# Performance work log

Measured on AMD Instinct MI355X. Metric: run time of the kernel, lower is better.

## Reference

```python
import jax, jax.numpy as jnp
import numpy as np

EPS = 1e-5


def conv2d(x, w, b, pad, mode='reflect'):
    # x: [B,C,H,W], w: [O,I,kh,kw]
    if pad > 0:
        x = jnp.pad(x, ((0, 0), (0, 0), (pad, pad), (pad, pad)), mode=mode)
    y = jax.lax.conv_general_dilated(x, w, (1, 1), 'VALID',
                                     dimension_numbers=('NCHW', 'OIHW', 'NCHW'))
    return y + b[None, :, None, None]


def inorm(x):
    # InstanceNorm2d, no affine (nn.InstanceNorm2d default)
    m = jnp.mean(x, axis=(2, 3), keepdims=True)
    v = jnp.mean((x - m) ** 2, axis=(2, 3), keepdims=True)
    return (x - m) * jax.lax.rsqrt(v + EPS)


def upsample2(x):
    # nn.Upsample(scale_factor=2), default nearest
    return jnp.repeat(jnp.repeat(x, 2, axis=2), 2, axis=3)


def bilinear_sample(img, py, px):
    # img [B,C,H,W]; py/px [B,H,W] float coords; zero padding outside bounds
    B, C, H, W = img.shape
    y0 = jnp.floor(py)
    x0 = jnp.floor(px)
    wy1 = (py - y0)[:, None]
    wx1 = (px - x0)[:, None]
    wy0 = 1.0 - wy1
    wx0 = 1.0 - wx1
    y0i = y0.astype(jnp.int32)
    x0i = x0.astype(jnp.int32)
    flat = img.reshape(B, C, H * W)

    def tap(yi, xi):
        valid = (yi >= 0) & (yi < H) & (xi >= 0) & (xi < W)
        idx = jnp.clip(yi, 0, H - 1) * W + jnp.clip(xi, 0, W - 1)
        g = jnp.take_along_axis(flat, idx.reshape(B, 1, H * W), axis=2).reshape(B, C, H, W)
        return g * valid[:, None]

    return (tap(y0i, x0i) * wy0 * wx0 + tap(y0i, x0i + 1) * wy0 * wx1 +
            tap(y0i + 1, x0i) * wy1 * wx0 + tap(y0i + 1, x0i + 1) * wy1 * wx1)


def mdcn(x, offset, mask, w, b):
    # modulated deformable conv v2: 3x3, stride 1, pad 1, 1 deformable group
    # offset [B,18,H,W] read as interleaved (dy,dx) per kernel tap; mask [B,9,H,W]
    B, C, H, W = x.shape
    off = offset.reshape(B, 9, 2, H, W)
    base_y = jnp.arange(H, dtype=x.dtype)[None, :, None]
    base_x = jnp.arange(W, dtype=x.dtype)[None, None, :]
    cols = []
    for k in range(9):
        ky, kx = k // 3 - 1, k % 3 - 1
        py = base_y + ky + off[:, k, 0]
        px = base_x + kx + off[:, k, 1]
        cols.append(bilinear_sample(x, py, px) * mask[:, k][:, None])
    col = jnp.stack(cols, axis=2)  # [B,C,9,H,W]
    out = jnp.einsum('bckhw,ock->bohw', col, w.reshape(w.shape[0], C, 9))
    return out + b[None, :, None, None]


def dcn_block(out, skip, off_w, off_b, w, b):
    # ModulatedDeformConvPack(double=True): offsets from concat, deform conv on skip
    dc = jnp.concatenate([out, skip], axis=1)
    om = conv2d(dc, off_w, off_b, 1, mode='constant')
    o1, o2, m = jnp.split(om, 3, axis=1)
    offset = jnp.concatenate([o1, o2], axis=1)
    pre = mdcn(skip, offset, jax.nn.sigmoid(m), w, b)
    return jnp.concatenate([pre, out], axis=1), offset


def decoder_fwd(x, skip1, skip2,
                rb0_w1, rb0_b1, rb0_w2, rb0_b2,
                rb1_w1, rb1_b1, rb1_w2, rb1_b2,
                conv1_w, conv1_b, conv3_w, conv3_b,
                conv5_w, conv5_b, conv6_w, conv6_b,
                dcn2_off_w, dcn2_off_b, dcn2_w, dcn2_b,
                dcn1_off_w, dcn1_off_b, dcn1_w, dcn1_b):
    out = x
    # i=0: ResBlocks (2 resblocks, 'in' norm, relu, reflect pad)
    for (w1, b1, w2, b2) in ((rb0_w1, rb0_b1, rb0_w2, rb0_b2),
                             (rb1_w1, rb1_b1, rb1_w2, rb1_b2)):
        h = jax.nn.relu(inorm(conv2d(out, w1, b1, 1)))
        out = out + inorm(conv2d(h, w2, b2, 1))
    # i=1: Conv2dBlock(256->256, 5x5)
    out = jax.nn.relu(inorm(conv2d(out, conv1_w, conv1_b, 2)))
    # dcn_2 hook (baseline_idx=2 -> dcn_idx=[1,3])
    out, offset2 = dcn_block(out, skip2, dcn2_off_w, dcn2_off_b, dcn2_w, dcn2_b)
    # i=2: upsample
    out = upsample2(out)
    # i=3: Conv2dBlock(512->128, 5x5)
    out = jax.nn.relu(inorm(conv2d(out, conv3_w, conv3_b, 2)))
    # dcn hook
    out, offset1 = dcn_block(out, skip1, dcn1_off_w, dcn1_off_b, dcn1_w, dcn1_b)
    # i=4: upsample
    out = upsample2(out)
    # i=5: Conv2dBlock(256->64, 5x5)
    out = jax.nn.relu(inorm(conv2d(out, conv5_w, conv5_b, 2)))
    # i=6: Conv2dBlock(64->3, 7x7, no norm, tanh)
    out = jnp.tanh(conv2d(out, conv6_w, conv6_b, 3))
    offset_sum = 0.5 * (jnp.mean(jnp.abs(offset1)) + jnp.mean(jnp.abs(offset2)))
    return out, offset_sum


def setup_inputs() -> dict:
    key = jax.random.key(0)
    ks = iter(jax.random.split(key, 48))

    def randn(shape, scale=1.0):
        return jax.random.normal(next(ks), shape, dtype=jnp.float32) * scale

    def conv_w(o, i, k, scale=1.0):
        return randn((o, i, k, k), scale / float(np.sqrt(i * k * k)))

    d = {}
    d['x'] = randn((8, 256, 32, 32))
    d['skip1'] = randn((8, 128, 64, 64))
    d['skip2'] = randn((8, 256, 32, 32))
    for r in range(2):
        d[f'rb{r}_w1'] = conv_w(256, 256, 3)
        d[f'rb{r}_b1'] = randn((256,), 0.01)
        d[f'rb{r}_w2'] = conv_w(256, 256, 3)
        d[f'rb{r}_b2'] = randn((256,), 0.01)
    d['conv1_w'] = conv_w(256, 256, 5); d['conv1_b'] = randn((256,), 0.01)
    d['conv3_w'] = conv_w(128, 512, 5); d['conv3_b'] = randn((128,), 0.01)
    d['conv5_w'] = conv_w(64, 256, 5); d['conv5_b'] = randn((64,), 0.01)
    d['conv6_w'] = conv_w(3, 64, 7); d['conv6_b'] = randn((3,), 0.01)
    d['dcn2_off_w'] = conv_w(27, 512, 3, 0.1); d['dcn2_off_b'] = randn((27,), 0.01)
    d['dcn2_w'] = conv_w(256, 256, 3); d['dcn2_b'] = randn((256,), 0.01)
    d['dcn1_off_w'] = conv_w(27, 256, 3, 0.1); d['dcn1_off_b'] = randn((27,), 0.01)
    d['dcn1_w'] = conv_w(128, 128, 3); d['dcn1_b'] = randn((128,), 0.01)
    return d


def reference(x, skip1, skip2,
              rb0_w1, rb0_b1, rb0_w2, rb0_b2,
              rb1_w1, rb1_b1, rb1_w2, rb1_b2,
              conv1_w, conv1_b, conv3_w, conv3_b,
              conv5_w, conv5_b, conv6_w, conv6_b,
              dcn2_off_w, dcn2_off_b, dcn2_w, dcn2_b,
              dcn1_off_w, dcn1_off_b, dcn1_w, dcn1_b):
    return decoder_fwd(x, skip1, skip2,
                       rb0_w1, rb0_b1, rb0_w2, rb0_b2,
                       rb1_w1, rb1_b1, rb1_w2, rb1_b2,
                       conv1_w, conv1_b, conv3_w, conv3_b,
                       conv5_w, conv5_b, conv6_w, conv6_b,
                       dcn2_off_w, dcn2_off_b, dcn2_w, dcn2_b,
                       dcn1_off_w, dcn1_off_b, dcn1_w, dcn1_b)
```

## Files before the change

### kernel.cpp

```cpp
#include <hip/hip_runtime.h>
#include <hip/hip_bf16.h>
#include <math.h>

typedef __hip_bfloat16 bf16;
typedef unsigned short u16;
typedef __attribute__((ext_vector_type(8))) short short8;
typedef __attribute__((ext_vector_type(4))) float f32x4;

__device__ __forceinline__ float LD(const float* p) { return *p; }
__device__ __forceinline__ float LD(const bf16* p)  { return __bfloat162float(*p); }
__device__ __forceinline__ void  ST(float* p, float v) { *p = v; }
__device__ __forceinline__ void  ST(bf16* p, float v)  { *p = __float2bfloat16(v); }
__device__ __forceinline__ u16   f2b(float v) { bf16 h = __float2bfloat16(v); return *reinterpret_cast<u16*>(&h); }
__device__ __forceinline__ float b2fu(u16 u) { bf16 h = *reinterpret_cast<bf16*>(&u); return __bfloat162float(h); }

__global__ __launch_bounds__(256) void copy_kernel(const float* __restrict__ in,
                                                   float* __restrict__ out, int n) {
    int i = blockIdx.x * blockDim.x + threadIdx.x;
    if (i < n) out[i] = in[i];
}

__global__ __launch_bounds__(256) void wsplit_kernel(const float* __restrict__ w,
                                                     u16* __restrict__ hi, u16* __restrict__ lo,
                                                     int O, int C, int KK)
{
    const int i = blockIdx.x * 256 + threadIdx.x;
    const int n = O * C * KK;
    if (i >= n) return;
    const int o = i / (C * KK);
    const int r = i - o * C * KK;
    const int c = r / KK;
    const int t = r - c * KK;
    const float v = w[i];
    const bf16 h = __float2bfloat16(v);
    const float hv = __bfloat162float(h);
    const bf16 l = __float2bfloat16(v - hv);
    const size_t dst = ((size_t)t * O + o) * C + c;
    hi[dst] = *(const u16*)&h;
    lo[dst] = *(const u16*)&l;
}

__global__ __launch_bounds__(256) void wsplit2_kernel(const float* __restrict__ w,
                                                      u16* __restrict__ hi, u16* __restrict__ lo,
                                                      int O, int C, int KK)
{
    const int i = blockIdx.x * 256 + threadIdx.x;
    const int n = O * C * KK;
    if (i >= n) return;
    const int o = i / (C * KK);
    const int r = i - o * C * KK;
    const int c = r / KK;
    const int t = r - c * KK;
    const float v = w[i];
    const bf16 h = __float2bfloat16(v);
    const float hv = __bfloat162float(h);
    const bf16 l = __float2bfloat16(v - hv);
    const int nch = C >> 5;
    const int cc = c >> 5, quad = (c >> 3) & 3, q = c & 7;
    const size_t dst = ((((size_t)t * nch + cc) * 4 + quad) * O + o) * 8 + q;
    hi[dst] = *(const u16*)&h;
    lo[dst] = *(const u16*)&l;
}

template<typename T1, typename T2, int K, bool UP, int EPI, bool ASPLIT,
         int NR, int NCOL, int MT, int MW>
__global__ __launch_bounds__(MW * 128) void conv_mfma3(
        const T1* __restrict__ src1, const T2* __restrict__ src2,
        int C1, int C,
        const u16* __restrict__ wth, const u16* __restrict__ wtl,
        const float* __restrict__ bias,
        void* __restrict__ outv, int O, int H, int W)
{
    constexpr int KK = K * K;
    constexpr int ATILE = NR * NCOL * 32;
    __shared__ __align__(16) u16 Ah[ATILE];
    __shared__ __align__(16) u16 Al[ASPLIT ? ATILE : 8];

    const int tid  = threadIdx.x;
    const int lane = tid & 63;
    const int wv   = tid >> 6;
    const int ln15 = lane & 15;
    const int quad = lane >> 4;
    const int mi = wv % MW, ni = wv / MW;
    const int b = blockIdx.y;
    const int p0 = blockIdx.x * (MT * 16 * MW);
    const int obase = blockIdx.z * 64;
    const int HW = H * W;
    const int SH = UP ? (H >> 1) : H;
    const int SW = UP ? (W >> 1) : W;
    const int SHW = SH * SW;
    const int PAD = K / 2;
    const int C2 = C - C1;
    const int nch = C >> 5;

    const int y0 = p0 / W;
    const int rbase = (y0 <= PAD) ? 0 : (UP ? ((y0 - PAD) >> 1) : (y0 - PAD));

    int rs[MT][K], cs[MT][K];
#pragma unroll
    for (int ms = 0; ms < MT; ++ms) {
        const int pm = p0 + mi * (MT * 16) + ms * 16 + ln15;
        const int ym = pm / W, xm = pm - ym * W;
#pragma unroll
        for (int tt = 0; tt < K; ++tt) {
            int yy = ym + tt - PAD;
            yy = yy < 0 ? -yy : yy; yy = yy >= H ? 2 * H - 2 - yy : yy;
            rs[ms][tt] = (UP ? (yy >> 1) : yy) - rbase;
            int xx = xm + tt - PAD;
            xx = xx < 0 ? -xx : xx; xx = xx >= W ? 2 * W - 2 - xx : xx;
            cs[ms][tt] = UP ? (xx >> 1) : xx;
        }
    }

    f32x4 acc[MT][2];
#pragma unroll
    for (int i = 0; i < MT; ++i)
#pragma unroll
        for (int j = 0; j < 2; ++j) acc[i][j] = (f32x4)0.f;

    for (int cc = 0; cc < nch; ++cc) {
        const int c0 = cc << 5;
        __syncthreads();
        for (int idx = tid; idx < NR * NCOL * 4; idx += MW * 128) {
            const int c_ = idx % NCOL;
            const int r_ = (idx / NCOL) % NR;
            const int cq = idx / (NCOL * NR);
            int rr = rbase + r_; rr = rr >= SH ? SH - 1 : rr;
            const int sidx = rr * SW + c_;
            short8 vh, vl;
#pragma unroll
            for (int q = 0; q < 8; ++q) {
                const int c = c0 + cq * 8 + q;
                float v;
                if (c < C1) v = LD(src1 + (size_t)(b * C1 + c) * SHW + sidx);
                else        v = LD(src2 + (size_t)(b * C2 + (c - C1)) * SHW + sidx);
                const u16 hv = f2b(v);
                vh[q] = (short)hv;
                if (ASPLIT) vl[q] = (short)f2b(v - b2fu(hv));
            }
            *(short8*)&Ah[idx * 8] = vh;
            if (ASPLIT) *(short8*)&Al[idx * 8] = vl;
        }
        __syncthreads();

#pragma unroll
        for (int t = 0; t < KK; ++t) {
            const int ty = t / K, tx = t - ty * K;
            const size_t wb0 = ((((size_t)t * nch + cc) * 4 + quad) * O
                                + obase + ni * 32 + ln15) * 8;
            const short8 b0h = *(const short8*)(wth + wb0);
            const short8 b1h = *(const short8*)(wth + wb0 + 128);
            const short8 b0l = *(const short8*)(wtl + wb0);
            const short8 b1l = *(const short8*)(wtl + wb0 + 128);
#pragma unroll
            for (int ms = 0; ms < MT; ++ms) {
                const int ao = ((quad * NR + rs[ms][ty]) * NCOL + cs[ms][tx]) * 8;
                const short8 a = *(const short8*)&Ah[ao];
                acc[ms][0] = __builtin_amdgcn_mfma_f32_16x16x32_bf16(a, b0h, acc[ms][0], 0, 0, 0);
                acc[ms][0] = __builtin_amdgcn_mfma_f32_16x16x32_bf16(a, b0l, acc[ms][0], 0, 0, 0);
                acc[ms][1] = __builtin_amdgcn_mfma_f32_16x16x32_bf16(a, b1h, acc[ms][1], 0, 0, 0);
                acc[ms][1] = __builtin_amdgcn_mfma_f32_16x16x32_bf16(a, b1l, acc[ms][1], 0, 0, 0);
                if (ASPLIT) {
                    const short8 al = *(const short8*)&Al[ao];
                    acc[ms][0] = __builtin_amdgcn_mfma_f32_16x16x32_bf16(al, b0h, acc[ms][0], 0, 0, 0);
                    acc[ms][1] = __builtin_amdgcn_mfma_f32_16x16x32_bf16(al, b1h, acc[ms][1], 0, 0, 0);
                }
            }
        }
    }

#pragma unroll
    for (int ms = 0; ms < MT; ++ms) {
#pragma unroll
        for (int ns = 0; ns < 2; ++ns) {
            const int o = obase + ni * 32 + ns * 16 + ln15;
            const float bv = bias[o];
            const f32x4 av = acc[ms][ns];
#pragma unroll
            for (int r = 0; r < 4; ++r) {
                const int pp = p0 + mi * (MT * 16) + ms * 16 + (quad << 2) + r;
                const float v = av[r] + bv;
                const size_t oidx = ((size_t)(b * O + o)) * HW + pp;
                if (EPI == 0) ((float*)outv)[oidx] = v;
                else          ((bf16*)outv)[oidx] = __float2bfloat16(v);
            }
        }
    }
}

template<typename OT, bool ASPLIT>
__global__ __launch_bounds__(256) void mdcn_mfma(
        const float* __restrict__ skip, const float* __restrict__ om,
        const u16* __restrict__ wth, const u16* __restrict__ wtl,
        const float* __restrict__ bias,
        OT* __restrict__ out, int C, int O, int H, int W)
{
    __shared__ float tpy[576], tpxs[576], tms[576];
    __shared__ __align__(16) u16 Ah[2][2048];
    __shared__ __align__(16) u16 Al[ASPLIT ? 2 : 1][2048];
    __shared__ __align__(16) u16 Bs[2][2][2048];

    const int tid = threadIdx.x;
    const int lane = tid & 63;
    const int wv = tid >> 6;
    const int ln15 = lane & 15;
    const int quad = lane >> 4;
    const int mi = wv & 1, ni = wv >> 1;
    const int b = blockIdx.y;
    const int p0 = blockIdx.x * 64;
    const int obase = blockIdx.z * 64;
    const int HW = H * W;
    const int nch = C >> 5;

    const float* omb = om + (size_t)b * 27 * HW;
    for (int i = tid; i < 576; i += 256) {
        const int k = i >> 6, px_ = i & 63;
        const int p = p0 + px_;
        const int y = p / W, x = p - y * W;
        const float dy = omb[(2 * k) * HW + p];
        const float dx = omb[(2 * k + 1) * HW + p];
        const float mk = 1.f / (1.f + expf(-omb[(18 + k) * HW + p]));
        float py = (float)(y + k / 3 - 1) + dy;
        float pxx = (float)(x + k % 3 - 1) + dx;
        py  = fminf(fmaxf(py, -2.f), (float)H + 1.f);
        pxx = fminf(fmaxf(pxx, -2.f), (float)W + 1.f);
        tpy[i] = py; tpxs[i] = pxx; tms[i] = mk;
    }
    __syncthreads();

    f32x4 acc[2][2];
#pragma unroll
    for (int i = 0; i < 2; ++i)
#pragma unroll
        for (int j = 0; j < 2; ++j) acc[i][j] = (f32x4)0.f;

    const float* xb = skip + (size_t)b * C * HW;
    const int ao0 = ((mi * 32 + ln15) * 4 + quad) * 8;
    const int ao1 = ((mi * 32 + 16 + ln15) * 4 + quad) * 8;
    const int bo0 = (quad * 64 + ni * 32 + ln15) * 8;
    const int bo1 = bo0 + 16 * 8;

    int chunk = 0;
    for (int cc = 0; cc < nch; ++cc) {
        const int c0c = cc << 5;
        const float* pb = xb + (size_t)(c0c + (wv << 3)) * HW;
        for (int k = 0; k < 9; ++k, ++chunk) {
            const int s = chunk & 1;
            const float py = tpy[k * 64 + lane], pxx = tpxs[k * 64 + lane], mk = tms[k * 64 + lane];
            const float y0f = floorf(py), x0f = floorf(pxx);
            const int y0 = (int)y0f, x0 = (int)x0f;
            const float wy1 = py - y0f, wx1 = pxx - x0f;
            const float wy0 = 1.f - wy1, wx0 = 1.f - wx1;
            const bool r0v = (y0 >= 0 && y0 < H), r1v = (y0 + 1 >= 0 && y0 + 1 < H);
            const bool c0v = (x0 >= 0 && x0 < W), c1v = (x0 + 1 >= 0 && x0 + 1 < W);
            const float w00 = (r0v && c0v) ? wy0 * wx0 * mk : 0.f;
            const float w01 = (r0v && c1v) ? wy0 * wx1 * mk : 0.f;
            const float w10 = (r1v && c0v) ? wy1 * wx0 * mk : 0.f;
            const float w11 = (r1v && c1v) ? wy1 * wx1 * mk : 0.f;
            const int i00 = (r0v ? y0 : 0) * W + (c0v ? x0 : 0);
            const int i01 = (r0v ? y0 : 0) * W + (c1v ? x0 + 1 : 0);
            const int i10 = (r1v ? y0 + 1 : 0) * W + (c0v ? x0 : 0);
            const int i11 = (r1v ? y0 + 1 : 0) * W + (c1v ? x0 + 1 : 0);
            {
                short8 vh, vl;
#pragma unroll
                for (int q = 0; q < 8; ++q) {
                    const float* pl = pb + (size_t)q * HW;
                    const float v = w00 * pl[i00] + w01 * pl[i01] + w10 * pl[i10] + w11 * pl[i11];
                    const u16 hv = f2b(v);
                    vh[q] = (short)hv;
                    if (ASPLIT) vl[q] = (short)f2b(v - b2fu(hv));
                }
                *(short8*)&Ah[s][(lane * 4 + wv) * 8] = vh;
                if (ASPLIT) *(short8*)&Al[s][(lane * 4 + wv) * 8] = vl;
            }
            {
                const size_t base = ((((size_t)k * nch + cc) * 4 + wv) * O + obase + lane) * 8;
                *(short8*)&Bs[s][0][tid * 8] = *(const short8*)(wth + base);
                *(short8*)&Bs[s][1][tid * 8] = *(const short8*)(wtl + base);
            }
            __syncthreads();
            const short8 a0 = *(const short8*)&Ah[s][ao0];
            const short8 a1 = *(const short8*)&Ah[s][ao1];
            const short8 b0h = *(const short8*)&Bs[s][0][bo0];
            const short8 b1h = *(const short8*)&Bs[s][0][bo1];
            const short8 b0l = *(const short8*)&Bs[s][1][bo0];
            const short8 b1l = *(const short8*)&Bs[s][1][bo1];
            acc[0][0] = __builtin_amdgcn_mfma_f32_16x16x32_bf16(a0, b0h, acc[0][0], 0, 0, 0);
            acc[0][0] = __builtin_amdgcn_mfma_f32_16x16x32_bf16(a0, b0l, acc[0][0], 0, 0, 0);
            acc[0][1] = __builtin_amdgcn_mfma_f32_16x16x32_bf16(a0, b1h, acc[0][1], 0, 0, 0);
            acc[0][1] = __builtin_amdgcn_mfma_f32_16x16x32_bf16(a0, b1l, acc[0][1], 0, 0, 0);
            acc[1][0] = __builtin_amdgcn_mfma_f32_16x16x32_bf16(a1, b0h, acc[1][0], 0, 0, 0);
            acc[1][0] = __builtin_amdgcn_mfma_f32_16x16x32_bf16(a1, b0l, acc[1][0], 0, 0, 0);
            acc[1][1] = __builtin_amdgcn_mfma_f32_16x16x32_bf16(a1, b1h, acc[1][1], 0, 0, 0);
            acc[1][1] = __builtin_amdgcn_mfma_f32_16x16x32_bf16(a1, b1l, acc[1][1], 0, 0, 0);
            if (ASPLIT) {
                const short8 a0l = *(const short8*)&Al[s][ao0];
                const short8 a1l = *(const short8*)&Al[s][ao1];
                acc[0][0] = __builtin_amdgcn_mfma_f32_16x16x32_bf16(a0l, b0h, acc[0][0], 0, 0, 0);
                acc[0][1] = __builtin_amdgcn_mfma_f32_16x16x32_bf16(a0l, b1h, acc[0][1], 0, 0, 0);
                acc[1][0] = __builtin_amdgcn_mfma_f32_16x16x32_bf16(a1l, b0h, acc[1][0], 0, 0, 0);
                acc[1][1] = __builtin_amdgcn_mfma_f32_16x16x32_bf16(a1l, b1h, acc[1][1], 0, 0, 0);
            }
        }
    }

#pragma unroll
    for (int ms = 0; ms < 2; ++ms) {
#pragma unroll
        for (int ns = 0; ns < 2; ++ns) {
            const int o = obase + ni * 32 + ns * 16 + ln15;
            const float bv = bias[o];
#pragma unroll
            for (int r = 0; r < 4; ++r) {
                const int pp = p0 + mi * 32 + ms * 16 + (quad << 2) + r;
                ST(out + ((size_t)(b * O + o)) * HW + pp, acc[ms][ns][r] + bv);
            }
        }
    }
}

template<typename T1, typename T2, int K, bool REFLECT, bool UP, int NTN, int EPI, bool ASPLIT>
__global__ __launch_bounds__(256) void conv_mfma(
        const T1* __restrict__ src1, const T2* __restrict__ src2,
        int C1, int C,
        const u16* __restrict__ wth, const u16* __restrict__ wtl,
        const float* __restrict__ bias,
        void* __restrict__ outv, int O, int H, int W)
{
    constexpr int KK = K * K;
    __shared__ __align__(16) u16 As[64 * 40];
    __shared__ __align__(16) u16 Alo[ASPLIT ? 64 * 40 : 8];
    __shared__ __align__(16) u16 Bh[NTN * 16 * 40];
    __shared__ __align__(16) u16 Bl[NTN * 16 * 40];

    const int tid  = threadIdx.x;
    const int wv   = tid >> 6;
    const int lane = tid & 63;
    const int ln15 = lane & 15;
    const int b    = blockIdx.y;
    const int p0   = blockIdx.x * 64;
    const int obase = blockIdx.z * (NTN * 16);
    const int HW = H * W;
    const int Hs = UP ? (H >> 1) : H;
    const int Ws = UP ? (W >> 1) : W;
    const int HsWs = Hs * Ws;
    const int PAD = K / 2;
    const int C2 = C - C1;
    const int m_stage = tid & 63;

    const int p = p0 + m_stage;
    const int y = p / W, x = p - y * W;
    int off[KK];
    float msk[KK];
#pragma unroll
    for (int ty = 0; ty < K; ++ty) {
#pragma unroll
        for (int tx = 0; tx < K; ++tx) {
            int yy = y + ty - PAD, xx = x + tx - PAD;
            bool vv = true;
            if (REFLECT) {
                yy = yy < 0 ? -yy : yy; yy = yy >= H ? 2 * H - 2 - yy : yy;
                xx = xx < 0 ? -xx : xx; xx = xx >= W ? 2 * W - 2 - xx : xx;
            } else {
                vv = (yy >= 0 && yy < H && xx >= 0 && xx < W);
                yy = yy < 0 ? 0 : (yy >= H ? H - 1 : yy);
                xx = xx < 0 ? 0 : (xx >= W ? W - 1 : xx);
            }
            off[ty * K + tx] = (UP ? (yy >> 1) : yy) * Ws + (UP ? (xx >> 1) : xx);
            msk[ty * K + tx] = vv ? 1.f : 0.f;
        }
    }

    f32x4 acc[NTN];
#pragma unroll
    for (int nt = 0; nt < NTN; ++nt) acc[nt] = (f32x4)0.f;

    const int aswz = (m_stage >> 3) & 3;
    const int awr  = m_stage * 40 + ((wv ^ aswz) << 3);
    const int arow = wv * 16 + ln15;
    const int ard  = arow * 40 + (((lane >> 4) ^ ((arow >> 3) & 3)) << 3);

    const int nch = C >> 5;
    for (int cc = 0; cc < nch; ++cc) {
        const int c0 = cc << 5;
        for (int t = 0; t < KK; ++t) {
            const int offt = off[t];
            const float mskt = msk[t];
            __syncthreads();
            {
                short8 avh, avl;
#pragma unroll
                for (int q = 0; q < 8; ++q) {
                    const int c = c0 + (wv << 3) + q;
                    float v;
                    if (c < C1) v = LD(src1 + ((size_t)(b * C1 + c)) * HsWs + offt);
                    else        v = LD(src2 + ((size_t)(b * C2 + (c - C1))) * HsWs + offt);
                    if (!REFLECT) v *= mskt;
                    const u16 hv = f2b(v);
                    avh[q] = (short)hv;
                    if (ASPLIT) avl[q] = (short)f2b(v - b2fu(hv));
                }
                *(short8*)&As[awr] = avh;
                if (ASPLIT) *(short8*)&Alo[awr] = avl;
            }
            for (int i = tid; i < NTN * 16 * 4; i += 256) {
                const int row = i >> 2, part = i & 3;
                int o = obase + row; if (o >= O) o = O - 1;
                const int pw = row * 40 + ((part ^ ((row >> 3) & 3)) << 3);
                const size_t wb = ((size_t)t * O + o) * C + c0 + (part << 3);
                *(short8*)&Bh[pw] = *(const short8*)(wth + wb);
                *(short8*)&Bl[pw] = *(const short8*)(wtl + wb);
            }
            __syncthreads();
            const short8 a = *(const short8*)&As[ard];
            short8 al;
            if (ASPLIT) al = *(const short8*)&Alo[ard];
#pragma unroll
            for (int nt = 0; nt < NTN; ++nt) {
                const int brow = nt * 16 + ln15;
                const int brd = brow * 40 + (((lane >> 4) ^ ((brow >> 3) & 3)) << 3);
                const short8 bh = *(const short8*)&Bh[brd];
                acc[nt] = __builtin_amdgcn_mfma_f32_16x16x32_bf16(a, bh, acc[nt], 0, 0, 0);
                const short8 bl = *(const short8*)&Bl[brd];
                acc[nt] = __builtin_amdgcn_mfma_f32_16x16x32_bf16(a, bl, acc[nt], 0, 0, 0);
                if (ASPLIT)
                    acc[nt] = __builtin_amdgcn_mfma_f32_16x16x32_bf16(al, bh, acc[nt], 0, 0, 0);
            }
        }
    }

#pragma unroll
    for (int nt = 0; nt < NTN; ++nt) {
        const int o = obase + nt * 16 + ln15;
        if (o < O) {
            const float bv = bias[o];
#pragma unroll
            for (int r = 0; r < 4; ++r) {
                const int pp = p0 + wv * 16 + ((lane >> 4) << 2) + r;
                const float v = acc[nt][r] + bv;
                const size_t oidx = ((size_t)(b * O + o)) * HW + pp;
                if (EPI == 0)      ((float*)outv)[oidx] = v;
                else if (EPI == 1) ((float*)outv)[oidx] = tanhf(v);
                else               ((bf16*)outv)[oidx] = __float2bfloat16(v);
            }
        }
    }
}

template<typename T>
__global__ __launch_bounds__(256) void inorm_kernel(T* __restrict__ buf,
                                                    float* __restrict__ resid,
                                                    int HW, int mode)
{
    __shared__ double sh0[256], sh1[256];
    const int pl = blockIdx.x;
    T* p = buf + (size_t)pl * HW;
    double s = 0.0, ss = 0.0;
    for (int i = threadIdx.x; i < HW; i += 256) {
        float v = LD(p + i);
        s += (double)v; ss += (double)v * (double)v;
    }
    sh0[threadIdx.x] = s; sh1[threadIdx.x] = ss;
    __syncthreads();
    for (int st = 128; st > 0; st >>= 1) {
        if (threadIdx.x < st) {
            sh0[threadIdx.x] += sh0[threadIdx.x + st];
            sh1[threadIdx.x] += sh1[threadIdx.x + st];
        }
        __syncthreads();
    }
    const double mean = sh0[0] / HW;
    const float m = (float)mean;
    const float var = (float)(sh1[0] / HW - mean * mean);
    const float inv = rsqrtf(var + 1e-5f);
    if (mode == 0) {
        for (int i = threadIdx.x; i < HW; i += 256) {
            float v = (LD(p + i) - m) * inv;
            ST(p + i, v > 0.f ? v : 0.f);
        }
    } else {
        float* r = resid + (size_t)pl * HW;
        for (int i = threadIdx.x; i < HW; i += 256)
            r[i] = r[i] + (LD(p + i) - m) * inv;
    }
}

__global__ void zero1_kernel(float* __restrict__ out) { if (threadIdx.x == 0) out[0] = 0.f; }

__global__ __launch_bounds__(256) void offsum_one(const float* __restrict__ om, int HW,
                                                  float* __restrict__ out)
{
    __shared__ double sh[256];
    const int n = 8 * 18 * HW;
    double s = 0.0;
    for (int i = blockIdx.x * 256 + threadIdx.x; i < n; i += gridDim.x * 256) {
        const int b = i / (18 * HW); const int r = i - b * 18 * HW;
        const int c = r / HW; const int p = r - c * HW;
        s += fabs((double)om[(size_t)(b * 27 + c) * HW + p]);
    }
    sh[threadIdx.x] = s;
    __syncthreads();
    for (int st = 128; st > 0; st >>= 1) {
        if (threadIdx.x < st) sh[threadIdx.x] += sh[threadIdx.x + st];
        __syncthreads();
    }
    if (threadIdx.x == 0) atomicAdd(out, (float)(0.5 * sh[0] / n));
}

extern "C" void kernel_launch(void* const* d_in, const int* in_sizes, int n_in,
                              void* d_out, int out_size, void* d_ws, size_t ws_size,
                              hipStream_t stream)
{
    if (n_in < 27) return;
    if (out_size < 393217) return;
    if (in_sizes[0] != 8 * 256 * 32 * 32) return;
    if (in_sizes[1] != 8 * 128 * 64 * 64) return;
    if (in_sizes[2] != 8 * 256 * 32 * 32) return;
    if (in_sizes[25] != 128 * 128 * 9) return;
    if (in_sizes[26] != 128) return;

    const float* x        = (const float*)d_in[0];
    const float* skip1    = (const float*)d_in[1];
    const float* skip2    = (const float*)d_in[2];
    const float* rbw[2][2] = {{(const float*)d_in[3], (const float*)d_in[5]},
                              {(const float*)d_in[7], (const float*)d_in[9]}};
    const float* rbb[2][2] = {{(const float*)d_in[4], (const float*)d_in[6]},
                              {(const float*)d_in[8], (const float*)d_in[10]}};
    const float* conv1_w = (const float*)d_in[11]; const float* conv1_b = (const float*)d_in[12];
    const float* conv3_w = (const float*)d_in[13]; const float* conv3_b = (const float*)d_in[14];
    const float* conv5_w = (const float*)d_in[15]; const float* conv5_b = (const float*)d_in[16];
    const float* conv6_w = (const float*)d_in[17]; const float* conv6_b = (const float*)d_in[18];
    const float* dcn2_off_w = (const float*)d_in[19]; const float* dcn2_off_b = (const float*)d_in[20];
    const float* dcn2_w = (const float*)d_in[21]; const float* dcn2_b = (const float*)d_in[22];
    const float* dcn1_off_w = (const float*)d_in[23]; const float* dcn1_off_b = (const float*)d_in[24];
    const float* dcn1_w = (const float*)d_in[25]; const float* dcn1_b = (const float*)d_in[26];

    float* outp = (float*)d_out;

    const size_t NEED_F32 = 9494528ull;
    if (ws_size < NEED_F32 * 4ull) return;

    float* ws = (float*)d_ws;
    const size_t NA = 2097152ull;
    float* A   = ws;
    float* Bb  = ws + NA;
    float* Tmp = ws + 2 * NA;
    float* om2 = ws + 3 * NA;
    float* om1 = om2 + 221184;
    bf16*  Fb  = (bf16*)(om1 + 884736);
    bf16*  Ib  = (bf16*)A;
    bf16*  Jb  = (bf16*)Bb;
    u16*   wm2h = (u16*)Tmp;
    u16*   wm2l = wm2h + 589824;
    u16*   wo2h = (u16*)(Tmp + 589824);
    u16*   wo2l = wo2h + 124416;
    u16*   wt3h = (u16*)Tmp;
    u16*   wt3l = wt3h + 25 * 128 * 512;
    u16*   wo1h = (u16*)Tmp;
    u16*   wo1l = wo1h + 62208;
    u16*   wm1h = (u16*)Bb;
    u16*   wm1l = wm1h + 147456;
    u16*   wt5h = (u16*)om1;
    u16*   wt5l = wt5h + 25 * 64 * 256;
    u16*   wt6h = (u16*)om2;
    u16*   wt6l = wt6h + 9408;
    u16*   wEh = (u16*)Fb;

    copy_kernel<<<8192, 256, 0, stream>>>(x, A, (int)NA);

    for (int r = 0; r < 2; ++r) {
        wsplit2_kernel<<<2304, 256, 0, stream>>>(rbw[r][0], wEh, wEh + 589824, 256, 256, 9);
        conv_mfma3<float, float, 3, false, 0, true, 4, 32, 2, 2><<<dim3(16, 8, 4), 256, 0, stream>>>(
            A, (const float*)nullptr, 256, 256, wEh, wEh + 589824, rbb[r][0], Bb, 256, 32, 32);
        inorm_kernel<float><<<2048, 256, 0, stream>>>(Bb, nullptr, 1024, 0);
        wsplit2_kernel<<<2304, 256, 0, stream>>>(rbw[r][1], wEh, wEh + 589824, 256, 256, 9);
        conv_mfma3<float, float, 3, false, 0, true, 4, 32, 2, 2><<<dim3(16, 8, 4), 256, 0, stream>>>(
            Bb, (const float*)nullptr, 256, 256, wEh, wEh + 589824, rbb[r][1], Tmp, 256, 32, 32);
        inorm_kernel<float><<<2048, 256, 0, stream>>>(Tmp, A, 1024, 1);
    }

    wsplit2_kernel<<<6400, 256, 0, stream>>>(conv1_w, wEh, wEh + 1638400, 256, 256, 25);
    conv_mfma3<float, float, 5, false, 0, true, 6, 32, 2, 2><<<dim3(16, 8, 4), 256, 0, stream>>>(
        A, (const float*)nullptr, 256, 256, wEh, wEh + 1638400, conv1_b, Bb, 256, 32, 32);
    inorm_kernel<float><<<2048, 256, 0, stream>>>(Bb, nullptr, 1024, 0);

    wsplit_kernel<<<486, 256, 0, stream>>>(dcn2_off_w, wo2h, wo2l, 27, 512, 9);
    conv_mfma<float, float, 3, false, false, 2, 0, false><<<dim3(16, 8, 1), 256, 0, stream>>>(
        Bb, skip2, 256, 512, wo2h, wo2l, dcn2_off_b, om2, 27, 32, 32);
    wsplit2_kernel<<<2304, 256, 0, stream>>>(dcn2_w, wm2h, wm2l, 256, 256, 9);
    mdcn_mfma<float, true><<<dim3(16, 8, 4), 256, 0, stream>>>(
        skip2, om2, wm2h, wm2l, dcn2_b, A, 256, 256, 32, 32);

    wsplit2_kernel<<<6400, 256, 0, stream>>>(conv3_w, wt3h, wt3l, 128, 512, 25);
    conv_mfma3<float, float, 5, true, 2, false, 4, 32, 4, 4><<<dim3(16, 8, 2), 512, 0, stream>>>(
        A, Bb, 256, 512, wt3h, wt3l, conv3_b, Fb, 128, 64, 64);
    inorm_kernel<bf16><<<1024, 256, 0, stream>>>(Fb, nullptr, 4096, 0);

    wsplit_kernel<<<243, 256, 0, stream>>>(dcn1_off_w, wo1h, wo1l, 27, 256, 9);
    conv_mfma<bf16, float, 3, false, false, 2, 0, false><<<dim3(64, 8, 1), 256, 0, stream>>>(
        Fb, skip1, 128, 256, wo1h, wo1l, dcn1_off_b, om1, 27, 64, 64);
    wsplit2_kernel<<<576, 256, 0, stream>>>(dcn1_w, wm1h, wm1l, 128, 128, 9);
    mdcn_mfma<bf16, true><<<dim3(64, 8, 2), 256, 0, stream>>>(
        skip1, om1, wm1h, wm1l, dcn1_b, Ib, 128, 128, 64, 64);

    zero1_kernel<<<1, 64, 0, stream>>>(outp + 393216);
    offsum_one<<<64, 256, 0, stream>>>(om1, 4096, outp + 393216);
    offsum_one<<<64, 256, 0, stream>>>(om2, 1024, outp + 393216);

    wsplit2_kernel<<<1600, 256, 0, stream>>>(conv5_w, wt5h, wt5l, 64, 256, 25);
    conv_mfma3<bf16, bf16, 5, true, 2, false, 3, 64, 4, 4><<<dim3(64, 8, 1), 512, 0, stream>>>(
        Ib, Fb, 128, 256, wt5h, wt5l, conv5_b, Jb, 64, 128, 128);
    inorm_kernel<bf16><<<512, 256, 0, stream>>>(Jb, nullptr, 16384, 0);

    wsplit_kernel<<<37, 256, 0, stream>>>(conv6_w, wt6h, wt6l, 3, 64, 49);
    conv_mfma<bf16, float, 7, true, false, 1, 1, false><<<dim3(256, 8, 1), 256, 0, stream>>>(
        Jb, (const float*)nullptr, 64, 64, wt6h, wt6l, conv6_b, (void*)outp, 3, 128, 128);
}
```

Before: 1.616 ms.

## Fold nearest-upsample into 5x5 conv weights with reflect-border correction terms

Adds conv_mfma5, which computes the upsample-then-5x5-reflect-pad conv directly on the low-resolution input. Vertically adjacent taps that read the same source row are pre-summed into combined weights per output row parity, and a separate correction path handles reflect-padding at the top and bottom borders. This cuts the vertical tap count and the staged input size for conv3 and conv5, and the A operand drops its low-precision split while summed weights keep hi/lo bf16. The mdcn kernel also gets XOR-swizzled LDS layout to avoid bank conflicts and a batch-fastest block remap, and the om2 offset-sum launch is moved earlier.

```diff
diff --git a/kernel.cpp b/kernel.cpp
--- a/kernel.cpp
+++ b/kernel.cpp
@@ -62,6 +62,40 @@
     lo[dst] = *(const u16*)&l;
 }
 
+__global__ __launch_bounds__(256) void wsplitL_kernel(const float* __restrict__ w,
+        u16* __restrict__ lh, u16* __restrict__ ll, u16* __restrict__ ch, int O, int C)
+{
+    const int i = blockIdx.x * 256 + threadIdx.x;
+    const int n = O * C * 50;
+    if (i >= n) return;
+    const int s = i / (O * C);
+    const int r = i - s * (O * C);
+    const int o = r / C;
+    const int c = r - o * C;
+    const size_t U = (size_t)C * O;
+    const int cc = c >> 5, quad = (c >> 3) & 3, q = c & 7;
+    const size_t din = (((size_t)cc * 4 + quad) * O + o) * 8 + q;
+    const float* wp = w + ((size_t)o * C + c) * 25;
+    if (s < 30) {
+        const int ry = s / 15, rem = s % 15, j = rem / 5, tx = rem % 5;
+        int ys, yn;
+        if (ry == 0) { ys = (j == 0) ? 0 : (j == 1) ? 2 : 4; yn = (j == 2) ? 1 : 2; }
+        else         { ys = (j == 0) ? 0 : (j == 1) ? 1 : 3; yn = (j == 0) ? 1 : 2; }
+        float v = 0.f;
+        for (int ty = ys; ty < ys + yn; ++ty) v += wp[ty * 5 + tx];
+        const bf16 h = __float2bfloat16(v);
+        const bf16 l = __float2bfloat16(v - __bfloat162float(h));
+        lh[(size_t)s * U + din] = *(const u16*)&h;
+        ll[(size_t)s * U + din] = *(const u16*)&l;
+    } else {
+        const int t = s - 30;
+        const int cidx = t / 5, tx = t - cidx * 5;
+        const int tyc = (cidx == 0) ? 0 : (cidx == 1) ? 1 : (cidx == 2) ? 3 : 4;
+        const bf16 h = __float2bfloat16(wp[tyc * 5 + tx]);
+        ch[(size_t)t * U + din] = *(const u16*)&h;
+    }
+}
+
 template<typename T1, typename T2, int K, bool UP, int EPI, bool ASPLIT,
          int NR, int NCOL, int MT, int MW>
 __global__ __launch_bounds__(MW * 128) void conv_mfma3(
@@ -188,6 +222,175 @@
     }
 }
 
+template<typename T1, typename T2, int NR, int NCOL, int MT, int MW>
+__global__ __launch_bounds__(MW * 128) void conv_mfma5(
+        const T1* __restrict__ src1, const T2* __restrict__ src2,
+        int C1, int C,
+        const u16* __restrict__ wLh, const u16* __restrict__ wLl,
+        const u16* __restrict__ wCh,
+        const float* __restrict__ bias,
+        bf16* __restrict__ out, int O, int H, int W)
+{
+    constexpr int NRR = NR + 1;
+    __shared__ __align__(16) u16 Ah[4 * NRR * NCOL * 8];
+
+    const int tid  = threadIdx.x;
+    const int lane = tid & 63;
+    const int wv   = tid >> 6;
+    const int ln15 = lane & 15;
+    const int quad = lane >> 4;
+    const int mi = wv % MW, ni = wv / MW;
+    const int b = blockIdx.y;
+    const int p0 = blockIdx.x * (MT * 16 * MW);
+    const int obase = blockIdx.z * 64;
+    const int HW = H * W;
+    const int SH = H >> 1, SW = W >> 1;
+    const int SHW = SH * SW;
+    const int C2 = C - C1;
+    const int nch = C >> 5;
+    const size_t U = (size_t)C * O;
+
+    const int y0 = p0 / W;
+    const int rbase = (y0 <= 2) ? 0 : ((y0 - 2) >> 1);
+
+    const int ym0 = (p0 + mi * (MT * 16)) / W;
+    const int ry = ym0 & 1;
+    const int uu = ym0 >> 1;
+    int r0 = uu - 1, r2 = uu + 1;
+    r0 = r0 < 0 ? 1 : r0;
+    r2 = r2 >= SH ? SH - 2 : r2;
+    const int rg0 = r0 - rbase, rg1 = uu - rbase, rg2 = r2 - rbase;
+
+    const bool isTopW = (ym0 <= 1), isBotW = (ym0 >= H - 2);
+    const bool isBorderW = isTopW || isBotW;
+    int cidx = 0;
+    if (isTopW) cidx = (ym0 == 0) ? 1 : 0;
+    if (isBotW) cidx = (ym0 == H - 2) ? 3 : 2;
+    const bool blkTop = (p0 == 0);
+    const bool blkBot = (p0 + MW * MT * 16 == HW);
+    const bool blkEdge = blkTop || blkBot;
+
+    int cs[MT][5];
+#pragma unroll
+    for (int ms = 0; ms < MT; ++ms) {
+        const int pm = p0 + mi * (MT * 16) + ms * 16 + ln15;
+        const int xm = pm % W;
+#pragma unroll
+        for (int tt = 0; tt < 5; ++tt) {
+            int xx = xm + tt - 2;
+            xx = xx < 0 ? -xx : xx; xx = xx >= W ? 2 * W - 2 - xx : xx;
+            cs[ms][tt] = xx >> 1;
+        }
+    }
+
+    f32x4 acc[MT][2];
+#pragma unroll
+    for (int i = 0; i < MT; ++i)
+#pragma unroll
+        for (int j = 0; j < 2; ++j) acc[i][j] = (f32x4)0.f;
+
+    for (int cc = 0; cc < nch; ++cc) {
+        const int c0 = cc << 5;
+        __syncthreads();
+        for (int idx = tid; idx < NR * NCOL * 4; idx += MW * 128) {
+            const int c_ = idx % NCOL;
+            const int r_ = (idx / NCOL) % NR;
+            const int cq = idx / (NCOL * NR);
+            int rr = rbase + r_; rr = rr >= SH ? SH - 1 : rr;
+            const int sidx = rr * SW + c_;
+            short8 vh;
+#pragma unroll
+            for (int q = 0; q < 8; ++q) {
+                const int c = c0 + cq * 8 + q;
+                float v;
+                if (c < C1) v = LD(src1 + (size_t)(b * C1 + c) * SHW + sidx);
+                else        v = LD(src2 + (size_t)(b * C2 + (c - C1)) * SHW + sidx);
+                vh[q] = (short)f2b(v);
+            }
+            *(short8*)&Ah[((cq * NRR + r_) * NCOL + c_) * 8] = vh;
+        }
+        if (blkEdge) {
+            const int ra = blkTop ? 0 : SH - 1;
+            const int rb2 = blkTop ? 1 : SH - 2;
+            for (int idx = tid; idx < NCOL * 4; idx += MW * 128) {
+                const int c_ = idx % NCOL;
+                const int cq = idx / NCOL;
+                short8 vh;
+#pragma unroll
+                for (int q = 0; q < 8; ++q) {
+                    const int c = c0 + cq * 8 + q;
+                    float va, vb;
+                    if (c < C1) {
+                        const size_t base = (size_t)(b * C1 + c) * SHW;
+                        va = LD(src1 + base + ra * SW + c_);
+                        vb = LD(src1 + base + rb2 * SW + c_);
+                    } else {
+                        const size_t base = (size_t)(b * C2 + (c - C1)) * SHW;
+                        va = LD(src2 + base + ra * SW + c_);
+                        vb = LD(src2 + base + rb2 * SW + c_);
+                    }
+                    vh[q] = (short)f2b(va - vb);
+                }
+                *(short8*)&Ah[((cq * NRR + NR) * NCOL + c_) * 8] = vh;
+            }
+        }
+        __syncthreads();
+
+        const size_t wq = ((size_t)(cc * 4 + quad) * O + obase + ni * 32 + ln15) * 8;
+#pragma unroll
+        for (int j = 0; j < 3; ++j) {
+            const int rgj = (j == 0) ? rg0 : (j == 1) ? rg1 : rg2;
+#pragma unroll
+            for (int tx = 0; tx < 5; ++tx) {
+                const size_t wb = (size_t)((ry * 3 + j) * 5 + tx) * U + wq;
+                const short8 b0h = *(const short8*)(wLh + wb);
+                const short8 b1h = *(const short8*)(wLh + wb + 128);
+                const short8 b0l = *(const short8*)(wLl + wb);
+                const short8 b1l = *(const short8*)(wLl + wb + 128);
+#pragma unroll
+                for (int ms = 0; ms < MT; ++ms) {
+                    const int ao = ((quad * NRR + rgj) * NCOL + cs[ms][tx]) * 8;
+                    const short8 a = *(const short8*)&Ah[ao];
+                    acc[ms][0] = __builtin_amdgcn_mfma_f32_16x16x32_bf16(a, b0h, acc[ms][0], 0, 0, 0);
+                    acc[ms][0] = __builtin_amdgcn_mfma_f32_16x16x32_bf16(a, b0l, acc[ms][0], 0, 0, 0);
+                    acc[ms][1] = __builtin_amdgcn_mfma_f32_16x16x32_bf16(a, b1h, acc[ms][1], 0, 0, 0);
+                    acc[ms][1] = __builtin_amdgcn_mfma_f32_16x16x32_bf16(a, b1l, acc[ms][1], 0, 0, 0);
+                }
+            }
+        }
+        if (isBorderW) {
+#pragma unroll
+            for (int tx = 0; tx < 5; ++tx) {
+                const size_t wb = (size_t)(cidx * 5 + tx) * U + wq;
+                const short8 b0 = *(const short8*)(wCh + wb);
+                const short8 b1 = *(const short8*)(wCh + wb + 128);
+#pragma unroll
+                for (int ms = 0; ms < MT; ++ms) {
+                    const int ao = ((quad * NRR + NR) * NCOL + cs[ms][tx]) * 8;
+                    const short8 a = *(const short8*)&Ah[ao];
+                    acc[ms][0] = __builtin_amdgcn_mfma_f32_16x16x32_bf16(a, b0, acc[ms][0], 0, 0, 0);
+                    acc[ms][1] = __builtin_amdgcn_mfma_f32_16x16x32_bf16(a, b1, acc[ms][1], 0, 0, 0);
+                }
+            }
+        }
+    }
+
+#pragma unroll
+    for (int ms = 0; ms < MT; ++ms) {
+#pragma unroll
+        for (int ns = 0; ns < 2; ++ns) {
+            const int o = obase + ni * 32 + ns * 16 + ln15;
+            const float bv = bias[o];
+            const f32x4 av = acc[ms][ns];
+#pragma unroll
+            for (int r = 0; r < 4; ++r) {
+                const int pp = p0 + mi * (MT * 16) + ms * 16 + (quad << 2) + r;
+                out[((size_t)(b * O + o)) * HW + pp] = __float2bfloat16(av[r] + bv);
+            }
+        }
+    }
+}
+
 template<typename OT, bool ASPLIT>
 __global__ __launch_bounds__(256) void mdcn_mfma(
         const float* __restrict__ skip, const float* __restrict__ om,
@@ -206,9 +409,11 @@
     const int ln15 = lane & 15;
     const int quad = lane >> 4;
     const int mi = wv & 1, ni = wv >> 1;
-    const int b = blockIdx.y;
-    const int p0 = blockIdx.x * 64;
-    const int obase = blockIdx.z * 64;
+    const int flat = blockIdx.x + gridDim.x * (blockIdx.y + 8 * blockIdx.z);
+    const int b = flat & 7;
+    const int rest = flat >> 3;
+    const int p0 = (rest % gridDim.x) * 64;
+    const int obase = (rest / gridDim.x) * 64;
     const int HW = H * W;
     const int nch = C >> 5;
 
@@ -235,8 +440,12 @@
         for (int j = 0; j < 2; ++j) acc[i][j] = (f32x4)0.f;
 
     const float* xb = skip + (size_t)b * C * HW;
-    const int ao0 = ((mi * 32 + ln15) * 4 + quad) * 8;
-    const int ao1 = ((mi * 32 + 16 + ln15) * 4 + quad) * 8;
+    const int swA = (lane >> 1) & 3;
+    const int awr = (lane * 4 + (wv ^ swA)) * 8;
+    const int pix0 = mi * 32 + ln15;
+    const int pix1 = pix0 + 16;
+    const int ao0 = (pix0 * 4 + (quad ^ ((pix0 >> 1) & 3))) * 8;
+    const int ao1 = (pix1 * 4 + (quad ^ ((pix1 >> 1) & 3))) * 8;
     const int bo0 = (quad * 64 + ni * 32 + ln15) * 8;
     const int bo1 = bo0 + 16 * 8;
 
@@ -271,8 +480,8 @@
                     vh[q] = (short)hv;
                     if (ASPLIT) vl[q] = (short)f2b(v - b2fu(hv));
                 }
-                *(short8*)&Ah[s][(lane * 4 + wv) * 8] = vh;
-                if (ASPLIT) *(short8*)&Al[s][(lane * 4 + wv) * 8] = vl;
+                *(short8*)&Ah[s][awr] = vh;
+                if (ASPLIT) *(short8*)&Al[s][awr] = vl;
             }
             {
                 const size_t base = ((((size_t)k * nch + cc) * 4 + wv) * O + obase + lane) * 8;
@@ -555,14 +764,16 @@
     u16*   wm2l = wm2h + 589824;
     u16*   wo2h = (u16*)(Tmp + 589824);
     u16*   wo2l = wo2h + 124416;
-    u16*   wt3h = (u16*)Tmp;
-    u16*   wt3l = wt3h + 25 * 128 * 512;
+    u16*   wL3h = (u16*)Tmp;
+    u16*   wL3l = wL3h + 30 * 65536;
+    u16*   wC3h = wL3l + 30 * 65536;
     u16*   wo1h = (u16*)Tmp;
     u16*   wo1l = wo1h + 62208;
     u16*   wm1h = (u16*)Bb;
     u16*   wm1l = wm1h + 147456;
-    u16*   wt5h = (u16*)om1;
-    u16*   wt5l = wt5h + 25 * 64 * 256;
+    u16*   wL5h = (u16*)om1;
+    u16*   wL5l = wL5h + 30 * 16384;
+    u16*   wC5h = wL5l + 30 * 16384;
     u16*   wt6h = (u16*)om2;
     u16*   wt6l = wt6h + 9408;
     u16*   wEh = (u16*)Fb;
@@ -592,9 +803,12 @@
     mdcn_mfma<float, true><<<dim3(16, 8, 4), 256, 0, stream>>>(
         skip2, om2, wm2h, wm2l, dcn2_b, A, 256, 256, 32, 32);
 
-    wsplit2_kernel<<<6400, 256, 0, stream>>>(conv3_w, wt3h, wt3l, 128, 512, 25);
-    conv_mfma3<float, float, 5, true, 2, false, 4, 32, 4, 4><<<dim3(16, 8, 2), 512, 0, stream>>>(
-        A, Bb, 256, 512, wt3h, wt3l, conv3_b, Fb, 128, 64, 64);
+    zero1_kernel<<<1, 64, 0, stream>>>(outp + 393216);
+    offsum_one<<<64, 256, 0, stream>>>(om2, 1024, outp + 393216);
+
+    wsplitL_kernel<<<12800, 256, 0, stream>>>(conv3_w, wL3h, wL3l, wC3h, 128, 512);
+    conv_mfma5<float, float, 4, 32, 4, 4><<<dim3(16, 8, 2), 512, 0, stream>>>(
+        A, Bb, 256, 512, wL3h, wL3l, wC3h, conv3_b, Fb, 128, 64, 64);
     inorm_kernel<bf16><<<1024, 256, 0, stream>>>(Fb, nullptr, 4096, 0);
 
     wsplit_kernel<<<243, 256, 0, stream>>>(dcn1_off_w, wo1h, wo1l, 27, 256, 9);
@@ -604,13 +818,11 @@
     mdcn_mfma<bf16, true><<<dim3(64, 8, 2), 256, 0, stream>>>(
         skip1, om1, wm1h, wm1l, dcn1_b, Ib, 128, 128, 64, 64);
 
-    zero1_kernel<<<1, 64, 0, stream>>>(outp + 393216);
     offsum_one<<<64, 256, 0, stream>>>(om1, 4096, outp + 393216);
-    offsum_one<<<64, 256, 0, stream>>>(om2, 1024, outp + 393216);
-
-    wsplit2_kernel<<<1600, 256, 0, stream>>>(conv5_w, wt5h, wt5l, 64, 256, 25);
-    conv_mfma3<bf16, bf16, 5, true, 2, false, 3, 64, 4, 4><<<dim3(64, 8, 1), 512, 0, stream>>>(
-        Ib, Fb, 128, 256, wt5h, wt5l, conv5_b, Jb, 64, 128, 128);
+
+    wsplitL_kernel<<<3200, 256, 0, stream>>>(conv5_w, wL5h, wL5l, wC5h, 64, 256);
+    conv_mfma5<bf16, bf16, 3, 64, 4, 4><<<dim3(64, 8, 1), 512, 0, stream>>>(
+        Ib, Fb, 128, 256, wL5h, wL5l, wC5h, conv5_b, Jb, 64, 128, 128);
     inorm_kernel<bf16><<<512, 256, 0, stream>>>(Jb, nullptr, 16384, 0);
 
     wsplit_kernel<<<37, 256, 0, stream>>>(conv6_w, wt6h, wt6l, 3, 64, 49);
```

Result: faster. 1.546 ms (-4.3%).
